# Kernel optimization log

Hardware: AMD Instinct MI355X
Metric: run time of the kernel (lower is better)

## Reference

```python
import jax, jax.numpy as jnp
import numpy as np

# ---- problem sizes / physics constants ----
N_EVENTS = 65536
N_OGATA = 64
NX, NB = 256, 256
LXMIN, LXMAX = float(np.log(1e-4)), 0.0            # log-x axis of OPE grids
LBMIN, LBMAX = float(np.log(1e-3)), float(np.log(50.0))  # log-bT axis of OPE grids
Q20 = 1.0            # reference scale Q0^2
G2 = 0.12            # CSS kernel coefficient: evolution = exp(-0.5*G2*bT^2*log(Q2/Q20))
M2 = 0.8803          # params.M2 (proton)
S_MAND = 140.0       # Mandelstam s (forward default)
ALPHA0 = 1.0 / 137.035999
ME2 = 0.000511 ** 2  # electron mass^2 for alpha_em running
# flavor order: u d s c cb sb db ub  (quark_charges_squared)
E2 = jnp.asarray([4/9, 1/9, 1/9, 4/9, 4/9, 1/9, 1/9, 4/9], dtype=jnp.float32)

# ---- Ogata quadrature nodes/weights for the J0 Hankel transform (precomputed, numpy) ----

def _trap(f, dth):
    return dth * (f.sum(-1) - 0.5 * (f[..., 0] + f[..., -1]))

def _J0(x, n=20001):
    th = np.linspace(0.0, np.pi, n)
    return _trap(np.cos(x[:, None] * np.sin(th)), th[1] - th[0]) / np.pi

def _J1(x, n=20001):
    th = np.linspace(0.0, np.pi, n)
    return _trap(np.cos(th - x[:, None] * np.sin(th)), th[1] - th[0]) / np.pi

def _ogata(N=N_OGATA, h=0.05):
    k = np.arange(1, N + 1)
    beta = (k - 0.25) * np.pi
    j0k = beta + 1.0 / (8 * beta) - 124.0 / (3 * (8 * beta) ** 3)  # J0 zeros (McMahon)
    r = j0k / np.pi
    t = h * r
    sh, ch = np.sinh(t), np.cosh(t)
    psi = t * np.tanh(0.5 * np.pi * sh)
    psip = np.tanh(0.5 * np.pi * sh) + t * (0.5 * np.pi * ch) / np.cosh(0.5 * np.pi * sh) ** 2
    u = np.pi * psi / h                      # quadrature nodes in v = qT*bT
    w = (2.0 / (np.pi * j0k)) / _J1(j0k) ** 2  # Y0(j0k)/J1(j0k) via Wronskian
    W = np.pi * w * _J0(u) * psip * u        # combined weight incl. J0 kernel and v Jacobian
    return u.astype(np.float32), W.astype(np.float32)


def setup_inputs() -> dict:
    key = jax.random.key(0)
    k0, k1, k2, k3 = jax.random.split(key, 4)
    u = jax.random.uniform(k0, (N_EVENTS, 4))
    y = 0.1 + 0.8 * u[:, 0]
    z = 0.2 + 0.6 * u[:, 1]
    Q = 1.2 + 1.8 * u[:, 2]
    x = Q ** 2 / ((S_MAND - M2) * y)          # physical DIS kinematics, x < 1
    PhT = (0.1 + 0.4 * u[:, 3]) * Q * z       # qT = PhT/z in [0.1Q, 0.5Q]
    events = jnp.stack([x, PhT, Q, z], axis=1).astype(jnp.float32)
    ope_pdf_grid = jax.random.uniform(k1, (8, NX, NB), dtype=jnp.float32)
    ope_ff_grid = jax.random.uniform(k2, (8, NX, NB), dtype=jnp.float32)
    fnp_params = 0.1 * jax.random.normal(k3, (4,), dtype=jnp.float32)
    un, Wn = _ogata()
    return {"events_tensor": events, "ope_pdf_grid": ope_pdf_grid,
            "ope_ff_grid": ope_ff_grid, "ogata_x": jnp.asarray(un),
            "ogata_w": jnp.asarray(Wn), "fnp_params": fnp_params}


def _interp2(grids, lx, lb):
    """Bilinear interp of grids (8,NX,NB) at (lx:(n,), lb:(n,K)) in log space -> (8,n,K)."""
    fx = jnp.clip((lx - LXMIN) / (LXMAX - LXMIN) * (NX - 1), 0.0, NX - 1 - 1e-4)
    fb = jnp.clip((lb - LBMIN) / (LBMAX - LBMIN) * (NB - 1), 0.0, NB - 1 - 1e-4)
    i0 = jnp.floor(fx).astype(jnp.int32)
    j0 = jnp.floor(fb).astype(jnp.int32)
    tx = (fx - i0)[None, :, None]   # (1,n,1)
    tb = (fb - j0)[None, :, :]      # (1,n,K)
    i0c = i0[:, None]               # (n,1) broadcast vs (n,K)
    g00 = grids[:, i0c, j0]
    g01 = grids[:, i0c, j0 + 1]
    g10 = grids[:, i0c + 1, j0]
    g11 = grids[:, i0c + 1, j0 + 1]
    return (1 - tx) * ((1 - tb) * g00 + tb * g01) + tx * ((1 - tb) * g10 + tb * g11)


def _forward(events, pdfg, ffg, ogx, ogw, fnp):
    x, PhT, Q, z = events[:, 0], events[:, 1], events[:, 2], events[:, 3]
    qT = PhT / z
    Q2 = Q * Q
    bT = ogx[None, :] / qT[:, None]                 # per-event ragged bT nodes (n,K)
    lb = jnp.log(bT)
    opepdf = _interp2(pdfg, jnp.log(x), lb)         # (8,n,K)
    opeff = _interp2(ffg, jnp.log(z), lb)           # (8,n,K)
    evo2 = jnp.exp(-G2 * bT ** 2 * jnp.log(Q2 / Q20)[:, None])  # evolution**2
    lam_p = jax.nn.softplus(fnp[0])
    lam_f = jax.nn.softplus(fnp[1])
    f_pdf = jnp.exp(-lam_p * bT ** 2 * (1.0 + jax.nn.sigmoid(fnp[2]) * jnp.log(1.0 / x))[:, None])
    f_ff = jnp.exp(-lam_f * (1.0 + jax.nn.sigmoid(fnp[3])) * bT ** 2 / (z ** 2)[:, None])
    # sum_flav e_q^2 * OPE_pdf * OPE_ff, then common evolution^2 * fNP factors
    integrand = jnp.einsum('f,fnk->nk', E2, opepdf * opeff) * evo2 * f_pdf * f_ff
    FUUT = (integrand * ogw[None, :]).sum(-1) / qT ** 2   # Ogata Hankel transform
    alpha = ALPHA0 / (1.0 - (ALPHA0 / (3.0 * jnp.pi)) * jnp.log(Q2 / ME2))
    gamma = 2.0 * M2 * x / Q
    y = Q2 / x / (S_MAND - M2)
    eps = (1.0 - y - 0.25 * gamma ** 2 * y ** 2) / (1.0 - y + 0.5 * y ** 2 + 0.25 * gamma ** 2 * y ** 2)
    pre = (8.0 * jnp.pi ** 2 * alpha ** 2 * z ** 2 * qT / x / Q ** 3
           * y ** 2 / 2.0 / (1.0 - eps) * (1.0 + gamma ** 2 / (2.0 * x)))
    return pre * FUUT


def reference(events_tensor, ope_pdf_grid, ope_ff_grid, ogata_x, ogata_w, fnp_params):
    return _forward(events_tensor, ope_pdf_grid, ope_ff_grid, ogata_x, ogata_w, fnp_params)
```

## Files before the change

kernel.cpp:

```cpp
#include <hip/hip_runtime.h>
#include <math.h>


namespace {
constexpr int   kNB    = 256;
constexpr int   kNX    = 256;
constexpr float kLXMIN = -9.210340371976182f;
constexpr float kLBMIN = -6.907755278982137f;
constexpr float kLBMAX =  3.912023005428146f;
constexpr float kScaleB = (float)(kNB - 1) / (kLBMAX - kLBMIN);
constexpr float kScaleX = (float)(kNX - 1) / (0.0f - kLXMIN);
constexpr float kG2    = 0.12f;
constexpr float kM2    = 0.8803f;
constexpr float kSmM2  = 140.0f - 0.8803f;
constexpr float kALPHA0 = 1.0f / 137.035999f;
constexpr float kLogME2 = -14.858672703081717f;
constexpr float kLog2E  = 1.4426950408889634f;
constexpr int   kGridElems = kNX * kNB;
}

typedef float    f32x4 __attribute__((ext_vector_type(4)));
typedef _Float16 f16x8 __attribute__((ext_vector_type(8)));

__device__ __forceinline__ float frcp(float x) { return __builtin_amdgcn_rcpf(x); }

#if __has_builtin(__builtin_amdgcn_exp2f)
__device__ __forceinline__ float fexp2(float x) { return __builtin_amdgcn_exp2f(x); }
#else
__device__ __forceinline__ float fexp2(float x) { return __expf(x * 0.6931471805599453f); }
#endif

__global__ __launch_bounds__(256) void prep_all(
    const float* __restrict__ pdfg, const float* __restrict__ ffg,
    const float* __restrict__ events,
    const float* __restrict__ ogx, const float* __restrict__ ogw,
    const float* __restrict__ fnp,
    _Float16* __restrict__ wpdf, _Float16* __restrict__ wff,
    float* __restrict__ evc, float* __restrict__ knode)
{
    const int idx = blockIdx.x * 256 + threadIdx.x;

    const float E2a[8] = {4.f/9, 1.f/9, 1.f/9, 4.f/9, 4.f/9, 1.f/9, 1.f/9, 4.f/9};
    f16x8 p, q;
    #pragma unroll
    for (int f = 0; f < 8; ++f) {
        p[f] = (_Float16)(pdfg[f * kGridElems + idx] * E2a[f]);
        q[f] = (_Float16)ffg[f * kGridElems + idx];
    }
    reinterpret_cast<f16x8*>(wpdf)[idx] = p;
    reinterpret_cast<f16x8*>(wff )[idx] = q;

    if (blockIdx.x == 0 && threadIdx.x < 64) {
        const float u = ogx[threadIdx.x];
        reinterpret_cast<f32x4*>(knode)[threadIdx.x] =
            (f32x4){__logf(u) * kScaleB, ogw[threadIdx.x], u * u, 0.0f};
    }

    const float4 e = reinterpret_cast<const float4*>(events)[idx];
    const float x = e.x, PhT = e.y, Q = e.z, z = e.w;

    const float lam_p = log1pf(__expf(fnp[0]));
    const float lam_f = log1pf(__expf(fnp[1]));
    const float sig2  = frcp(1.0f + __expf(-fnp[2]));
    const float sig3  = frcp(1.0f + __expf(-fnp[3]));

    const float rz  = frcp(z);
    const float qT  = PhT * rz;
    const float rqT = z * frcp(PhT);
    const float Q2  = Q * Q;
    const float lx  = __logf(x);
    const float lz  = __logf(z);
    const float lqT = __logf(qT);
    const float lQ2 = 2.0f * __logf(Q);

    const float fbofs = (-lqT - kLBMIN) * kScaleB;

    float fxp = (lx - kLXMIN) * kScaleX;
    fxp = fminf(fmaxf(fxp, 0.0f), (float)(kNX - 1) - 1e-4f);
    const int   i0p = (int)fxp;
    const float txp = fxp - (float)i0p;

    float fxf = (lz - kLXMIN) * kScaleX;
    fxf = fminf(fmaxf(fxf, 0.0f), (float)(kNX - 1) - 1e-4f);
    const int   i0f = (int)fxf;
    const float txf = fxf - (float)i0f;

    const float D  = kG2 * lQ2
                   + lam_p * (1.0f - sig2 * lx)
                   + lam_f * (1.0f + sig3) * (rz * rz);
    const float nD2 = -(rqT * rqT) * D * kLog2E;

    const float alpha = kALPHA0 *
        frcp(1.0f - kALPHA0 / (3.0f * (float)M_PI) * (lQ2 - kLogME2));
    const float rQ    = frcp(Q);
    const float rx    = frcp(x);
    const float gamma = 2.0f * kM2 * x * rQ;
    const float y     = Q2 * rx * (1.0f / kSmM2);
    const float g2y2  = 0.25f * gamma * gamma * y * y;
    const float eps   = (1.0f - y - g2y2) *
                        frcp(1.0f - y + 0.5f * y * y + g2y2);
    const float pre   = 8.0f * (float)(M_PI * M_PI) * alpha * alpha
                      * z * z * qT * rx * (rQ * rQ * rQ)
                      * y * y * 0.5f * frcp(1.0f - eps)
                      * fmaf(gamma * gamma * 0.5f, rx, 1.0f);
    const float scale = pre * rqT * rqT;

    const int prowByte = i0p * kNB * 16;
    const int frowByte = i0f * kNB * 16;

    f32x4* dst = reinterpret_cast<f32x4*>(evc + (size_t)idx * 8);
    dst[0] = (f32x4){fbofs, nD2, scale, txp};
    dst[1] = (f32x4){txf, __int_as_float(prowByte), __int_as_float(frowByte), 0.0f};
}

__global__ __launch_bounds__(256) void sidis_fwd11(
    const float* __restrict__ evc,
    const _Float16* __restrict__ wpdf,
    const _Float16* __restrict__ wff,
    const float* __restrict__ knode,
    float* __restrict__ out)
{
    const int lane = threadIdx.x & 63;
    const int wslt = threadIdx.x >> 6;
    const int grp  = lane >> 3;
    const int k    = lane & 7;
    const int ev   = blockIdx.x * 32 + wslt * 8 + grp;

    const f32x4 c1 = reinterpret_cast<const f32x4*>(evc)[ev * 2];
    const f32x4 kn = reinterpret_cast<const f32x4*>(knode)[k];

    const float ex2 = kn.z * c1.y;
    float val = 0.0f;

    if (ex2 > -140.0f) {
        const f32x4 c2 = reinterpret_cast<const f32x4*>(evc)[ev * 2 + 1];
        const _Float16 txph = (_Float16)c1.w;
        const _Float16 txfh = (_Float16)c2.x;
        const int prowByte = __float_as_int(c2.y);
        const int frowByte = __float_as_int(c2.z);

        float fb = kn.x + c1.x;
        fb = fminf(fmaxf(fb, 0.0f), (float)(kNB - 1) - 1e-4f);
        const int j0 = (int)fb;
        const _Float16 tbh = (_Float16)(fb - (float)j0);
        const int cell = j0 << 4;

        const char* pp0 = reinterpret_cast<const char*>(wpdf) + prowByte;
        const char* pp1 = pp0 + kNB * 16;
        const char* fp0 = reinterpret_cast<const char*>(wff) + frowByte;
        const char* fp1 = fp0 + kNB * 16;

        const f16x8 p00 = *reinterpret_cast<const f16x8*>(pp0 + cell);
        const f16x8 p01 = *reinterpret_cast<const f16x8*>(pp0 + cell + 16);
        const f16x8 p10 = *reinterpret_cast<const f16x8*>(pp1 + cell);
        const f16x8 p11 = *reinterpret_cast<const f16x8*>(pp1 + cell + 16);
        const f16x8 q00 = *reinterpret_cast<const f16x8*>(fp0 + cell);
        const f16x8 q01 = *reinterpret_cast<const f16x8*>(fp0 + cell + 16);
        const f16x8 q10 = *reinterpret_cast<const f16x8*>(fp1 + cell);
        const f16x8 q11 = *reinterpret_cast<const f16x8*>(fp1 + cell + 16);

        const f16x8 pr0 = p00 + tbh * (p01 - p00);
        const f16x8 pr1 = p10 + tbh * (p11 - p10);
        const f16x8 pvh = pr0 + txph * (pr1 - pr0);
        const f16x8 qr0 = q00 + tbh * (q01 - q00);
        const f16x8 qr1 = q10 + tbh * (q11 - q10);
        const f16x8 fvh = qr0 + txfh * (qr1 - qr0);

        const f32x4 pv_lo = {(float)pvh[0], (float)pvh[1], (float)pvh[2], (float)pvh[3]};
        const f32x4 pv_hi = {(float)pvh[4], (float)pvh[5], (float)pvh[6], (float)pvh[7]};
        const f32x4 fv_lo = {(float)fvh[0], (float)fvh[1], (float)fvh[2], (float)fvh[3]};
        const f32x4 fv_hi = {(float)fvh[4], (float)fvh[5], (float)fvh[6], (float)fvh[7]};

        const f32x4 acc = pv_lo * fv_lo + pv_hi * fv_hi;
        const float s = (acc.x + acc.y) + (acc.z + acc.w);

        val = s * fexp2(ex2) * kn.y;
    }

    val += __shfl_down(val, 4, 8);
    val += __shfl_down(val, 2, 8);
    val += __shfl_down(val, 1, 8);

    if (k == 0)
        out[ev] = c1.z * val;
}

__global__ __launch_bounds__(256) void sidis_fwd_direct(
    const float* __restrict__ events,
    const float* __restrict__ pdfg,
    const float* __restrict__ ffg,
    const float* __restrict__ ogx,
    const float* __restrict__ ogw,
    const float* __restrict__ fnp,
    float* __restrict__ out)
{
    const int lane = threadIdx.x & 63;
    const int ev   = (blockIdx.x << 2) + (threadIdx.x >> 6);

    const float4 e = reinterpret_cast<const float4*>(events)[ev];
    const float x = e.x, PhT = e.y, Q = e.z, z = e.w;
    const float qT = PhT / z;
    const float Q2 = Q * Q;

    const float lam_p = log1pf(__expf(fnp[0]));
    const float lam_f = log1pf(__expf(fnp[1]));
    const float sig2  = 1.0f / (1.0f + __expf(-fnp[2]));
    const float sig3  = 1.0f / (1.0f + __expf(-fnp[3]));

    const float u_k = ogx[lane];
    const float w_k = ogw[lane];
    const float bT  = u_k / qT;
    const float lb  = __logf(bT);

    float fb = (lb - kLBMIN) * kScaleB;
    fb = fminf(fmaxf(fb, 0.0f), (float)(kNB - 1) - 1e-4f);
    const int   j0 = (int)fb;
    const float tb = fb - (float)j0;

    const float lx = __logf(x);
    float fxp = (lx - kLXMIN) * kScaleX;
    fxp = fminf(fmaxf(fxp, 0.0f), (float)(kNX - 1) - 1e-4f);
    const int   i0p = (int)fxp;
    const float txp = fxp - (float)i0p;

    const float lz = __logf(z);
    float fxf = (lz - kLXMIN) * kScaleX;
    fxf = fminf(fmaxf(fxf, 0.0f), (float)(kNX - 1) - 1e-4f);
    const int   i0f = (int)fxf;
    const float txf = fxf - (float)i0f;

    const float* pbase = pdfg + i0p * kNB + j0;
    const float* fbase = ffg  + i0f * kNB + j0;
    const float E2a[8] = {4.f/9, 1.f/9, 1.f/9, 4.f/9, 4.f/9, 1.f/9, 1.f/9, 4.f/9};

    float s = 0.0f;
    #pragma unroll
    for (int f = 0; f < 8; ++f) {
        const float* gp = pbase + f * kGridElems;
        const float p00 = gp[0], p01 = gp[1], p10 = gp[kNB], p11 = gp[kNB + 1];
        const float* gf = fbase + f * kGridElems;
        const float q00 = gf[0], q01 = gf[1], q10 = gf[kNB], q11 = gf[kNB + 1];
        const float pv = (1.0f - txp) * ((1.0f - tb) * p00 + tb * p01)
                       +          txp * ((1.0f - tb) * p10 + tb * p11);
        const float fv = (1.0f - txf) * ((1.0f - tb) * q00 + tb * q01)
                       +          txf * ((1.0f - tb) * q10 + tb * q11);
        s += E2a[f] * pv * fv;
    }

    const float bT2 = bT * bT;
    const float lQ2 = __logf(Q2);
    const float expo = -bT2 * (kG2 * lQ2
                               + lam_p * (1.0f - sig2 * lx)
                               + lam_f * (1.0f + sig3) / (z * z));
    float val = s * __expf(expo) * w_k;

    #pragma unroll
    for (int off = 32; off > 0; off >>= 1)
        val += __shfl_down(val, off, 64);

    if (lane == 0) {
        const float FUUT  = val / (qT * qT);
        const float alpha = kALPHA0 /
            (1.0f - kALPHA0 / (3.0f * (float)M_PI) * (lQ2 - kLogME2));
        const float gamma = 2.0f * kM2 * x / Q;
        const float y     = Q2 / (x * kSmM2);
        const float g2y2  = 0.25f * gamma * gamma * y * y;
        const float eps   = (1.0f - y - g2y2) /
                            (1.0f - y + 0.5f * y * y + g2y2);
        const float pre   = 8.0f * (float)(M_PI * M_PI) * alpha * alpha
                          * z * z * qT / x / (Q2 * Q)
                          * y * y * 0.5f / (1.0f - eps)
                          * (1.0f + gamma * gamma / (2.0f * x));
        out[ev] = pre * FUUT;
    }
}

extern "C" void kernel_launch(void* const* d_in, const int* in_sizes, int n_in,
                              void* d_out, int out_size, void* d_ws, size_t ws_size,
                              hipStream_t stream) {
    const float* events = (const float*)d_in[0];
    const float* pdfg   = (const float*)d_in[1];
    const float* ffg    = (const float*)d_in[2];
    const float* ogx    = (const float*)d_in[3];
    const float* ogw    = (const float*)d_in[4];
    const float* fnp    = (const float*)d_in[5];
    float* out = (float*)d_out;

    const int nev = in_sizes[0] / 4;

    const size_t gbytes = (size_t)kGridElems * 8 * sizeof(_Float16);
    const size_t ebytes = (size_t)nev * 8 * sizeof(float);
    const size_t kbytes = 4096;
    const size_t need = 2 * gbytes + ebytes + kbytes;

    if (ws_size >= need && nev == kGridElems) {
        char* base = (char*)d_ws;
        _Float16* wpdf  = (_Float16*)base;
        _Float16* wff   = (_Float16*)(base + gbytes);
        float*    evc   = (float*)(base + 2 * gbytes);
        float*    knode = (float*)(base + 2 * gbytes + ebytes);

        prep_all<<<kGridElems / 256, 256, 0, stream>>>(
            pdfg, ffg, events, ogx, ogw, fnp, wpdf, wff, evc, knode);
        sidis_fwd11<<<nev / 32, 256, 0, stream>>>(evc, wpdf, wff, knode, out);
    } else {
        sidis_fwd_direct<<<nev / 4, 256, 0, stream>>>(events, pdfg, ffg,
                                                      ogx, ogw, fnp, out);
    }
}
```

Before: 72.84 us.

## Fuse per-event precompute into main kernel, drop event workspace buffer

Moves the per-event kinematic precompute (logs, interpolation indices, damping exponent, prefactor) out of the prep kernel and into the main quadrature kernel, so each event is computed from the raw event tensor. This removes the 2 MB event-constants workspace write and reread. The fNP scalar transforms are still computed once, in block 0 of the prep kernel. In exchange, all 8 lanes of each event group redo the logs and reciprocals, and the prefactor is evaluated in the reduction lane, which adds ALU work to the main kernel.

```diff
diff --git a/kernel.cpp b/kernel.cpp
--- a/kernel.cpp
+++ b/kernel.cpp
@@ -30,13 +30,12 @@
 __device__ __forceinline__ float fexp2(float x) { return __expf(x * 0.6931471805599453f); }
 #endif
 
-__global__ __launch_bounds__(256) void prep_all(
+__global__ __launch_bounds__(256) void prep_grid(
     const float* __restrict__ pdfg, const float* __restrict__ ffg,
-    const float* __restrict__ events,
     const float* __restrict__ ogx, const float* __restrict__ ogw,
     const float* __restrict__ fnp,
     _Float16* __restrict__ wpdf, _Float16* __restrict__ wff,
-    float* __restrict__ evc, float* __restrict__ knode)
+    float* __restrict__ knode)
 {
     const int idx = blockIdx.x * 256 + threadIdx.x;
 
@@ -50,71 +49,24 @@
     reinterpret_cast<f16x8*>(wpdf)[idx] = p;
     reinterpret_cast<f16x8*>(wff )[idx] = q;
 
-    if (blockIdx.x == 0 && threadIdx.x < 64) {
-        const float u = ogx[threadIdx.x];
-        reinterpret_cast<f32x4*>(knode)[threadIdx.x] =
-            (f32x4){__logf(u) * kScaleB, ogw[threadIdx.x], u * u, 0.0f};
-    }
-
-    const float4 e = reinterpret_cast<const float4*>(events)[idx];
-    const float x = e.x, PhT = e.y, Q = e.z, z = e.w;
-
-    const float lam_p = log1pf(__expf(fnp[0]));
-    const float lam_f = log1pf(__expf(fnp[1]));
-    const float sig2  = frcp(1.0f + __expf(-fnp[2]));
-    const float sig3  = frcp(1.0f + __expf(-fnp[3]));
-
-    const float rz  = frcp(z);
-    const float qT  = PhT * rz;
-    const float rqT = z * frcp(PhT);
-    const float Q2  = Q * Q;
-    const float lx  = __logf(x);
-    const float lz  = __logf(z);
-    const float lqT = __logf(qT);
-    const float lQ2 = 2.0f * __logf(Q);
-
-    const float fbofs = (-lqT - kLBMIN) * kScaleB;
-
-    float fxp = (lx - kLXMIN) * kScaleX;
-    fxp = fminf(fmaxf(fxp, 0.0f), (float)(kNX - 1) - 1e-4f);
-    const int   i0p = (int)fxp;
-    const float txp = fxp - (float)i0p;
-
-    float fxf = (lz - kLXMIN) * kScaleX;
-    fxf = fminf(fmaxf(fxf, 0.0f), (float)(kNX - 1) - 1e-4f);
-    const int   i0f = (int)fxf;
-    const float txf = fxf - (float)i0f;
-
-    const float D  = kG2 * lQ2
-                   + lam_p * (1.0f - sig2 * lx)
-                   + lam_f * (1.0f + sig3) * (rz * rz);
-    const float nD2 = -(rqT * rqT) * D * kLog2E;
-
-    const float alpha = kALPHA0 *
-        frcp(1.0f - kALPHA0 / (3.0f * (float)M_PI) * (lQ2 - kLogME2));
-    const float rQ    = frcp(Q);
-    const float rx    = frcp(x);
-    const float gamma = 2.0f * kM2 * x * rQ;
-    const float y     = Q2 * rx * (1.0f / kSmM2);
-    const float g2y2  = 0.25f * gamma * gamma * y * y;
-    const float eps   = (1.0f - y - g2y2) *
-                        frcp(1.0f - y + 0.5f * y * y + g2y2);
-    const float pre   = 8.0f * (float)(M_PI * M_PI) * alpha * alpha
-                      * z * z * qT * rx * (rQ * rQ * rQ)
-                      * y * y * 0.5f * frcp(1.0f - eps)
-                      * fmaf(gamma * gamma * 0.5f, rx, 1.0f);
-    const float scale = pre * rqT * rqT;
-
-    const int prowByte = i0p * kNB * 16;
-    const int frowByte = i0f * kNB * 16;
-
-    f32x4* dst = reinterpret_cast<f32x4*>(evc + (size_t)idx * 8);
-    dst[0] = (f32x4){fbofs, nD2, scale, txp};
-    dst[1] = (f32x4){txf, __int_as_float(prowByte), __int_as_float(frowByte), 0.0f};
-}
-
-__global__ __launch_bounds__(256) void sidis_fwd11(
-    const float* __restrict__ evc,
+    if (blockIdx.x == 0) {
+        if (threadIdx.x < 64) {
+            const float u = ogx[threadIdx.x];
+            reinterpret_cast<f32x4*>(knode)[threadIdx.x] =
+                (f32x4){__logf(u) * kScaleB, ogw[threadIdx.x], u * u, 0.0f};
+        } else if (threadIdx.x == 64) {
+            const float lam_p = log1pf(__expf(fnp[0]));
+            const float lam_f = log1pf(__expf(fnp[1]));
+            const float sig2  = frcp(1.0f + __expf(-fnp[2]));
+            const float sig3  = frcp(1.0f + __expf(-fnp[3]));
+            *reinterpret_cast<f32x4*>(knode + 256) =
+                (f32x4){lam_p, lam_f, sig2, sig3};
+        }
+    }
+}
+
+__global__ __launch_bounds__(256) void sidis_fwd12(
+    const float* __restrict__ events,
     const _Float16* __restrict__ wpdf,
     const _Float16* __restrict__ wff,
     const float* __restrict__ knode,
@@ -126,28 +78,51 @@
     const int k    = lane & 7;
     const int ev   = blockIdx.x * 32 + wslt * 8 + grp;
 
-    const f32x4 c1 = reinterpret_cast<const f32x4*>(evc)[ev * 2];
+    const float4 e = reinterpret_cast<const float4*>(events)[ev];
+    const float x = e.x, PhT = e.y, Q = e.z, z = e.w;
+
     const f32x4 kn = reinterpret_cast<const f32x4*>(knode)[k];
-
-    const float ex2 = kn.z * c1.y;
+    const f32x4 fc = *reinterpret_cast<const f32x4*>(knode + 256);
+
+    const float rz  = frcp(z);
+    const float qT  = PhT * rz;
+    const float rqT = z * frcp(PhT);
+    const float lx  = __logf(x);
+    const float lz  = __logf(z);
+    const float lqT = __logf(qT);
+    const float lQ2 = 2.0f * __logf(Q);
+    const float Q2  = Q * Q;
+
+    const float fbofs = (-lqT - kLBMIN) * kScaleB;
+
+    const float D  = kG2 * lQ2
+                   + fc.x * (1.0f - fc.z * lx)
+                   + fc.y * (1.0f + fc.w) * (rz * rz);
+    const float nD2 = -(rqT * rqT) * D * kLog2E;
+    const float ex2 = kn.z * nD2;
+
     float val = 0.0f;
 
     if (ex2 > -140.0f) {
-        const f32x4 c2 = reinterpret_cast<const f32x4*>(evc)[ev * 2 + 1];
-        const _Float16 txph = (_Float16)c1.w;
-        const _Float16 txfh = (_Float16)c2.x;
-        const int prowByte = __float_as_int(c2.y);
-        const int frowByte = __float_as_int(c2.z);
-
-        float fb = kn.x + c1.x;
+        float fxp = (lx - kLXMIN) * kScaleX;
+        fxp = fminf(fmaxf(fxp, 0.0f), (float)(kNX - 1) - 1e-4f);
+        const int      i0p  = (int)fxp;
+        const _Float16 txph = (_Float16)(fxp - (float)i0p);
+
+        float fxf = (lz - kLXMIN) * kScaleX;
+        fxf = fminf(fmaxf(fxf, 0.0f), (float)(kNX - 1) - 1e-4f);
+        const int      i0f  = (int)fxf;
+        const _Float16 txfh = (_Float16)(fxf - (float)i0f);
+
+        float fb = kn.x + fbofs;
         fb = fminf(fmaxf(fb, 0.0f), (float)(kNB - 1) - 1e-4f);
         const int j0 = (int)fb;
         const _Float16 tbh = (_Float16)(fb - (float)j0);
         const int cell = j0 << 4;
 
-        const char* pp0 = reinterpret_cast<const char*>(wpdf) + prowByte;
+        const char* pp0 = reinterpret_cast<const char*>(wpdf) + i0p * (kNB * 16);
         const char* pp1 = pp0 + kNB * 16;
-        const char* fp0 = reinterpret_cast<const char*>(wff) + frowByte;
+        const char* fp0 = reinterpret_cast<const char*>(wff) + i0f * (kNB * 16);
         const char* fp1 = fp0 + kNB * 16;
 
         const f16x8 p00 = *reinterpret_cast<const f16x8*>(pp0 + cell);
@@ -181,8 +156,22 @@
     val += __shfl_down(val, 2, 8);
     val += __shfl_down(val, 1, 8);
 
-    if (k == 0)
-        out[ev] = c1.z * val;
+    if (k == 0) {
+        const float alpha = kALPHA0 *
+            frcp(1.0f - kALPHA0 / (3.0f * (float)M_PI) * (lQ2 - kLogME2));
+        const float rQ    = frcp(Q);
+        const float rx    = frcp(x);
+        const float gamma = 2.0f * kM2 * x * rQ;
+        const float y     = Q2 * rx * (1.0f / kSmM2);
+        const float g2y2  = 0.25f * gamma * gamma * y * y;
+        const float eps   = (1.0f - y - g2y2) *
+                            frcp(1.0f - y + 0.5f * y * y + g2y2);
+        const float pre   = 8.0f * (float)(M_PI * M_PI) * alpha * alpha
+                          * z * z * qT * rx * (rQ * rQ * rQ)
+                          * y * y * 0.5f * frcp(1.0f - eps)
+                          * fmaf(gamma * gamma * 0.5f, rx, 1.0f);
+        out[ev] = pre * rqT * rqT * val;
+    }
 }
 
 __global__ __launch_bounds__(256) void sidis_fwd_direct(
@@ -289,20 +278,18 @@
     const int nev = in_sizes[0] / 4;
 
     const size_t gbytes = (size_t)kGridElems * 8 * sizeof(_Float16);
-    const size_t ebytes = (size_t)nev * 8 * sizeof(float);
     const size_t kbytes = 4096;
-    const size_t need = 2 * gbytes + ebytes + kbytes;
+    const size_t need = 2 * gbytes + kbytes;
 
     if (ws_size >= need && nev == kGridElems) {
         char* base = (char*)d_ws;
         _Float16* wpdf  = (_Float16*)base;
         _Float16* wff   = (_Float16*)(base + gbytes);
-        float*    evc   = (float*)(base + 2 * gbytes);
-        float*    knode = (float*)(base + 2 * gbytes + ebytes);
-
-        prep_all<<<kGridElems / 256, 256, 0, stream>>>(
-            pdfg, ffg, events, ogx, ogw, fnp, wpdf, wff, evc, knode);
-        sidis_fwd11<<<nev / 32, 256, 0, stream>>>(evc, wpdf, wff, knode, out);
+        float*    knode = (float*)(base + 2 * gbytes);
+
+        prep_grid<<<kGridElems / 256, 256, 0, stream>>>(
+            pdfg, ffg, ogx, ogw, fnp, wpdf, wff, knode);
+        sidis_fwd12<<<nev / 32, 256, 0, stream>>>(events, wpdf, wff, knode, out);
     } else {
         sidis_fwd_direct<<<nev / 4, 256, 0, stream>>>(events, pdfg, ffg,
                                                       ogx, ogw, fnp, out);
```

New measurement: 71.03 us. 1.03x faster.
